# Kernel optimization log

Measured on AMD Instinct MI355X. Metric: run time of the kernel, lower is better.

Reference implementation:

```python
import jax, jax.numpy as jnp
import numpy as np

MAX_SHIFT = 4.0  # init max_shift; stored shifts are pre-divided by it
Q = 3            # Maclaurin order


def setup_inputs() -> dict:
    key = jax.random.key(0)
    k1, k2, k3, k4 = jax.random.split(key, 4)
    x = jax.random.normal(k1, (16, 64, 112, 112), jnp.float32)
    # weights: (out_channels, q*in_channels, k, k)
    weights = jax.random.normal(k2, (128, 192, 3, 3), jnp.float32) * 0.05
    bias = jax.random.normal(k3, (128,), jnp.float32) * 0.05
    # stored shifts buffer: uniform(-max_shift, max_shift) then /= max_shift -> [-1, 1]
    shifts = jax.random.uniform(k4, (64, 2), jnp.float32, -1.0, 1.0)
    return {"x": x, "weights": weights, "bias": bias, "shifts": shifts}


def _shift_one_channel(xc, sx, sy):
    """Bilinear translate one channel by (sx, sy) pixels, zero padding.
    Equivalent to F.affine_grid(identity + [sx/(W/2), sy/(H/2)]) + grid_sample
    (align_corners=False): out[n, i, j] = x[n, i + sy, j + sx] (bilinear).
    xc: (N, H, W)."""
    N, H, W = xc.shape
    jx = jnp.arange(W, dtype=xc.dtype) + sx  # sampled x coord per output col
    iy = jnp.arange(H, dtype=xc.dtype) + sy  # sampled y coord per output row
    x0f = jnp.floor(jx)
    y0f = jnp.floor(iy)
    wx = jx - x0f  # (W,)
    wy = iy - y0f  # (H,)
    x0 = x0f.astype(jnp.int32)
    y0 = y0f.astype(jnp.int32)

    def gather(yi, xi):
        vy = (yi >= 0) & (yi < H)
        vx = (xi >= 0) & (xi < W)
        yc = jnp.clip(yi, 0, H - 1)
        xcl = jnp.clip(xi, 0, W - 1)
        v = xc[:, yc, :][:, :, xcl]  # (N, H, W)
        return v * (vy[:, None] & vx[None, :]).astype(xc.dtype)

    return ((1 - wy)[:, None] * (1 - wx)[None, :] * gather(y0, x0)
            + (1 - wy)[:, None] * wx[None, :] * gather(y0, x0 + 1)
            + wy[:, None] * (1 - wx)[None, :] * gather(y0 + 1, x0)
            + wy[:, None] * wx[None, :] * gather(y0 + 1, x0 + 1))


def reference(x, weights, bias, shifts):
    s = shifts * MAX_SHIFT  # pixel shifts, (C_in, 2) = (sx, sy)
    # per-channel bilinear shift (vmap over channel axis)
    shifted = jax.vmap(_shift_one_channel, in_axes=(1, 0, 0), out_axes=1)(
        x, s[:, 0], s[:, 1])  # (N, C, H, W)
    # Maclaurin powers concatenated along channels: (N, q*C, H, W)
    y = jnp.concatenate([shifted ** i for i in range(1, Q + 1)], axis=1)
    out = jax.lax.conv_general_dilated(
        y, weights, window_strides=(1, 1), padding=[(1, 1), (1, 1)],
        dimension_numbers=("NCHW", "OIHW", "NCHW"))
    return out + bias[None, :, None, None]
```

## Files before the change

kernel.cpp:

```cpp
#include <hip/hip_runtime.h>
#include <hip/hip_bf16.h>

typedef __bf16 bf16x8 __attribute__((ext_vector_type(8)));
typedef float  f32x4  __attribute__((ext_vector_type(4)));

#define H_DIM 112
#define W_DIM 112
#define CIN 64
#define CMID 192
#define COUT 128
#define NB 16

__device__ __forceinline__ void dma16(const void* g, void* l) {
    __builtin_amdgcn_global_load_lds(
        (const __attribute__((address_space(1))) unsigned*)g,
        (__attribute__((address_space(3))) unsigned*)l, 16, 0, 0);
}

__global__ __launch_bounds__(256) void repack_w_kernel(
    const float* __restrict__ w, __hip_bfloat16* __restrict__ wr)
{
    int idx = blockIdx.x * 256 + threadIdx.x;
    if (idx < 9 * COUT * CMID) {
        int ci  = idx % CMID;
        int t   = idx / CMID;
        int co  = t % COUT;
        int khw = t / COUT;
        wr[idx] = __float2bfloat16(w[(co * CMID + ci) * 9 + khw]);
    }
}

__global__ __launch_bounds__(256) void shift_pow_kernel(
    const float* __restrict__ x, const float* __restrict__ shifts,
    __hip_bfloat16* __restrict__ y)
{
    __shared__ __align__(16) float xs[64 * 116];
    __shared__ __align__(16) __hip_bfloat16 tile[112 * 104];
    __shared__ float4 prm[32];

    const int tid = threadIdx.x;
    const int h   = blockIdx.x;
    const int cb  = blockIdx.y * 32;
    const int n   = blockIdx.z;

    if (tid < 32) {
        float sx = shifts[2 * (cb + tid)]     * 4.0f;
        float sy = shifts[2 * (cb + tid) + 1] * 4.0f;
        float fx = floorf(sx), fy = floorf(sy);
        prm[tid] = make_float4(fx, fy, sx - fx, sy - fy);
    }
    __syncthreads();

    #pragma unroll
    for (int k = 0; k < 7; ++k) {
        int i     = k * 256 + tid;
        int rowid = i / 28;
        int part  = i - rowid * 28;
        int c = rowid >> 1, t = rowid & 1;
        int iy = (int)prm[c].y;
        int r  = h + iy + t;
        bool valid = (unsigned)r < (unsigned)H_DIM;
        int rr = min(max(r, 0), H_DIM - 1);
        float4 v = ((const float4*)(
            x + ((size_t)(n * CIN + cb + c) * H_DIM + rr) * W_DIM))[part];
        if (!valid) v = make_float4(0.f, 0.f, 0.f, 0.f);
        *(float4*)&xs[rowid * 116 + part * 4] = v;
    }
    __syncthreads();

    #pragma unroll
    for (int k = 0; k < 14; ++k) {
        int i  = k * 256 + tid;
        int c  = i / 112;
        int px = i - c * 112;
        float4 p = prm[c];
        int ix = (int)p.x;
        float wx = p.z, wy = p.w;
        int q0 = px + ix, q1 = q0 + 1;
        float f0 = ((unsigned)q0 < (unsigned)W_DIM) ? 1.f : 0.f;
        float f1 = ((unsigned)q1 < (unsigned)W_DIM) ? 1.f : 0.f;
        int a0 = min(max(q0, 0), W_DIM - 1);
        int a1 = min(max(q1, 0), W_DIM - 1);
        const float* r0 = &xs[(2 * c) * 116];
        const float* r1 = &xs[(2 * c + 1) * 116];
        float top = (1.f - wx) * f0 * r0[a0] + wx * f1 * r0[a1];
        float bot = (1.f - wx) * f0 * r1[a0] + wx * f1 * r1[a1];
        float v  = (1.f - wy) * top + wy * bot;
        float v2 = v * v, v3 = v2 * v;
        __hip_bfloat16* tp = &tile[px * 104];
        tp[c]      = __float2bfloat16(v);
        tp[c + 32] = __float2bfloat16(v2);
        tp[c + 64] = __float2bfloat16(v3);
    }
    __syncthreads();

    const float4* tl4 = (const float4*)tile;
    float4* yo4 = (float4*)(y + ((size_t)(n * H_DIM + h) * W_DIM) * CMID);
    const int cbd4 = cb >> 3;
    #pragma unroll
    for (int k = 0; k < 6; ++k) {
        int i = k * 256 + tid;
        if (i < 1344) {
            int px  = i / 12;
            int cp4 = i - px * 12;
            int chunk = cp4 >> 2, e4 = cp4 & 3;
            yo4[px * 24 + chunk * 8 + cbd4 + e4] = tl4[px * 13 + cp4];
        }
    }
}

#define YSTR_E 104
#define BUF_E  12288

__global__ __launch_bounds__(256, 3) void conv_kernel(
    const __bf16* __restrict__ y,
    const __bf16* __restrict__ wr,
    const float* __restrict__ bias,
    float* __restrict__ out)
{
    __shared__ __align__(16) __bf16 ybuf[2][BUF_E];

    const int tid  = threadIdx.x;
    const int lane = tid & 63;
    const int wid  = tid >> 6;
    const int m    = lane & 15;
    const int quad = lane >> 4;

    const int h = blockIdx.x;
    const int n = blockIdx.y;

    if (tid < 208) {
        int b    = tid >= 104;
        int r    = tid - b * 104;
        int slot = (r >= 52) ? 113 : 0;
        int dw   = (r >= 52) ? r - 52 : r;
        ((unsigned*)&ybuf[b][0])[slot * 52 + dw] = 0u;
    }

    int dj[6];
    #pragma unroll
    for (int j = 0; j < 6; ++j) {
        int t = 4 * j + wid;
        int o = 208 + 1024 * t + 16 * lane;
        int slot = o / 208;
        int rem  = o - slot * 208;
        dj[j] = (t < 23 && rem < 192 && slot <= 112)
                    ? ((slot - 1) * 384 + rem) : -1;
    }

    f32x4 acc[2][7];
    #pragma unroll
    for (int mt = 0; mt < 2; ++mt)
        #pragma unroll
        for (int nt = 0; nt < 7; ++nt)
            #pragma unroll
            for (int r = 0; r < 4; ++r) acc[mt][nt][r] = 0.0f;

    const char* ybase = (const char*)y + (size_t)n * (H_DIM * W_DIM * CMID * 2);

    const int f = (h == 0)         ? 2 : 0;
    const int l = (h == H_DIM - 1) ? 3 : 5;

    {
        int row = h + (f >> 1) - 1, half = f & 1;
        const char* src = ybase + (size_t)row * (W_DIM * CMID * 2) + half * 192;
        char* lb = (char*)&ybuf[0][0];
        #pragma unroll
        for (int j = 0; j < 6; ++j) {
            int t = 4 * j + wid;
            if (dj[j] >= 0) dma16(src + dj[j], lb + 208 + 1024 * t);
        }
    }
    __syncthreads();

    int buf = 0;
    for (int s = f; s <= l; ++s) {
        if (s < l) {
            int row = h + ((s + 1) >> 1) - 1, half = (s + 1) & 1;
            const char* src = ybase + (size_t)row * (W_DIM * CMID * 2) + half * 192;
            char* lb = (char*)&ybuf[buf ^ 1][0];
            #pragma unroll
            for (int j = 0; j < 6; ++j) {
                int t = 4 * j + wid;
                if (dj[j] >= 0) dma16(src + dj[j], lb + 208 + 1024 * t);
            }
        }

        const int kh = s >> 1, half = s & 1;
        const __bf16* lbase = &ybuf[buf][m * YSTR_E + quad * 8];
        #pragma unroll
        for (int c3 = 0; c3 < 3; ++c3) {
            const int ci = half * 96 + c3 * 32 + quad * 8;
            bf16x8 af[3][2];
            #pragma unroll
            for (int kw = 0; kw < 3; ++kw)
                #pragma unroll
                for (int mt = 0; mt < 2; ++mt)
                    af[kw][mt] = *(const bf16x8*)(
                        wr + (size_t)((kh * 3 + kw) * COUT + wid * 32 + mt * 16 + m) * CMID + ci);
            #pragma unroll
            for (int kw = 0; kw < 3; ++kw) {
                bf16x8 bfr[7];
                #pragma unroll
                for (int nt = 0; nt < 7; ++nt)
                    bfr[nt] = *(const bf16x8*)(lbase + (nt * 16 + kw) * YSTR_E + c3 * 32);
                #pragma unroll
                for (int nt = 0; nt < 7; ++nt) {
                    acc[0][nt] = __builtin_amdgcn_mfma_f32_16x16x32_bf16(
                        af[kw][0], bfr[nt], acc[0][nt], 0, 0, 0);
                    acc[1][nt] = __builtin_amdgcn_mfma_f32_16x16x32_bf16(
                        af[kw][1], bfr[nt], acc[1][nt], 0, 0, 0);
                }
            }
        }
        __syncthreads();
        buf ^= 1;
    }

    #pragma unroll
    for (int mt = 0; mt < 2; ++mt) {
        const int co0 = wid * 32 + mt * 16 + quad * 4;
        float bv[4];
        #pragma unroll
        for (int rr = 0; rr < 4; ++rr) bv[rr] = bias[co0 + rr];
        #pragma unroll
        for (int nt = 0; nt < 7; ++nt) {
            int j = nt * 16 + m;
            #pragma unroll
            for (int rr = 0; rr < 4; ++rr) {
                out[(((size_t)n * COUT + co0 + rr) * H_DIM + h) * W_DIM + j] =
                    acc[mt][nt][rr] + bv[rr];
            }
        }
    }
}

extern "C" void kernel_launch(void* const* d_in, const int* in_sizes, int n_in,
                              void* d_out, int out_size, void* d_ws, size_t ws_size,
                              hipStream_t stream) {
    const float* x      = (const float*)d_in[0];
    const float* w      = (const float*)d_in[1];
    const float* bias   = (const float*)d_in[2];
    const float* shifts = (const float*)d_in[3];
    float* out = (float*)d_out;

    __hip_bfloat16* y  = (__hip_bfloat16*)d_ws;
    __hip_bfloat16* wr = (__hip_bfloat16*)((char*)d_ws + 77070336);

    repack_w_kernel<<<dim3((9 * COUT * CMID + 255) / 256), 256, 0, stream>>>(w, wr);
    shift_pow_kernel<<<dim3(H_DIM, 2, NB), 256, 0, stream>>>(x, shifts, y);
    conv_kernel<<<dim3(H_DIM, NB), 256, 0, stream>>>(
        (const __bf16*)y, (const __bf16*)wr, bias, out);
}
```

Measured before the change: 293.6 us.

## Software-pipeline LDS fragment loads with MFMA and remap blocks across XCDs

The conv inner loop now loads all 18 weight fragments up front and double-buffers the B-fragment LDS reads, prefetching the next (c3,kw) group while the current group's MFMAs run. sched_group_barrier hints interleave the ds_reads with the MFMAs. Launch bounds drop from 3 to 2 waves per EU minimum to make room for the larger register footprint. The grid is flattened and swizzled so consecutive rows of the same image land on the same XCD for L2 reuse. The cost is lower occupancy from the extra registers.

```diff
diff --git a/kernel.cpp b/kernel.cpp
--- a/kernel.cpp
+++ b/kernel.cpp
@@ -112,7 +112,34 @@
 #define YSTR_E 104
 #define BUF_E  12288
 
-__global__ __launch_bounds__(256, 3) void conv_kernel(
+#define CONV_GROUP(G, CUR, NXT) do {                                          \
+    const int c3_ = (G) / 3, kw_ = (G) % 3;                                   \
+    if ((G) < 8) {                                                            \
+        const int c3n_ = ((G) + 1) / 3, kwn_ = ((G) + 1) % 3;                 \
+        _Pragma("unroll")                                                     \
+        for (int nt = 0; nt < 7; ++nt)                                        \
+            NXT[nt] = *(const bf16x8*)(lbase +                                \
+                (nt * 16 + kwn_) * YSTR_E + c3n_ * 32);                       \
+    }                                                                         \
+    _Pragma("unroll")                                                         \
+    for (int nt = 0; nt < 7; ++nt) {                                          \
+        acc[0][nt] = __builtin_amdgcn_mfma_f32_16x16x32_bf16(                 \
+            af[c3_][kw_][0], CUR[nt], acc[0][nt], 0, 0, 0);                   \
+        acc[1][nt] = __builtin_amdgcn_mfma_f32_16x16x32_bf16(                 \
+            af[c3_][kw_][1], CUR[nt], acc[1][nt], 0, 0, 0);                   \
+    }                                                                         \
+    if ((G) < 8) {                                                            \
+        _Pragma("unroll")                                                     \
+        for (int k_ = 0; k_ < 7; ++k_) {                                      \
+            __builtin_amdgcn_sched_group_barrier(0x100, 1, 0);   \
+            __builtin_amdgcn_sched_group_barrier(0x008, 2, 0);    \
+        }                                                                     \
+    } else {                                                                  \
+        __builtin_amdgcn_sched_group_barrier(0x008, 14, 0);                   \
+    }                                                                         \
+} while (0)
+
+__global__ __launch_bounds__(256, 2) void conv_kernel(
     const __bf16* __restrict__ y,
     const __bf16* __restrict__ wr,
     const float* __restrict__ bias,
@@ -126,8 +153,10 @@
     const int m    = lane & 15;
     const int quad = lane >> 4;
 
-    const int h = blockIdx.x;
-    const int n = blockIdx.y;
+    const int bid = blockIdx.x;
+    const int id  = (bid & 7) * 224 + (bid >> 3);
+    const int n   = id / H_DIM;
+    const int h   = id - n * H_DIM;
 
     if (tid < 208) {
         int b    = tid >= 104;
@@ -188,31 +217,34 @@
 
         const int kh = s >> 1, half = s & 1;
         const __bf16* lbase = &ybuf[buf][m * YSTR_E + quad * 8];
-        #pragma unroll
-        for (int c3 = 0; c3 < 3; ++c3) {
-            const int ci = half * 96 + c3 * 32 + quad * 8;
-            bf16x8 af[3][2];
+
+        bf16x8 af[3][3][2];
+        #pragma unroll
+        for (int c3 = 0; c3 < 3; ++c3)
             #pragma unroll
             for (int kw = 0; kw < 3; ++kw)
                 #pragma unroll
                 for (int mt = 0; mt < 2; ++mt)
-                    af[kw][mt] = *(const bf16x8*)(
-                        wr + (size_t)((kh * 3 + kw) * COUT + wid * 32 + mt * 16 + m) * CMID + ci);
-            #pragma unroll
-            for (int kw = 0; kw < 3; ++kw) {
-                bf16x8 bfr[7];
-                #pragma unroll
-                for (int nt = 0; nt < 7; ++nt)
-                    bfr[nt] = *(const bf16x8*)(lbase + (nt * 16 + kw) * YSTR_E + c3 * 32);
-                #pragma unroll
-                for (int nt = 0; nt < 7; ++nt) {
-                    acc[0][nt] = __builtin_amdgcn_mfma_f32_16x16x32_bf16(
-                        af[kw][0], bfr[nt], acc[0][nt], 0, 0, 0);
-                    acc[1][nt] = __builtin_amdgcn_mfma_f32_16x16x32_bf16(
-                        af[kw][1], bfr[nt], acc[1][nt], 0, 0, 0);
-                }
-            }
-        }
+                    af[c3][kw][mt] = *(const bf16x8*)(
+                        wr + (size_t)((kh * 3 + kw) * COUT + wid * 32 + mt * 16 + m) * CMID
+                           + half * 96 + c3 * 32 + quad * 8);
+
+        bf16x8 bA[7], bB[7];
+        #pragma unroll
+        for (int nt = 0; nt < 7; ++nt)
+            bA[nt] = *(const bf16x8*)(lbase + (nt * 16 + 0) * YSTR_E + 0 * 32);
+        __builtin_amdgcn_sched_group_barrier(0x100, 7, 0);
+
+        CONV_GROUP(0, bA, bB);
+        CONV_GROUP(1, bB, bA);
+        CONV_GROUP(2, bA, bB);
+        CONV_GROUP(3, bB, bA);
+        CONV_GROUP(4, bA, bB);
+        CONV_GROUP(5, bB, bA);
+        CONV_GROUP(6, bA, bB);
+        CONV_GROUP(7, bB, bA);
+        CONV_GROUP(8, bA, bB);
+
         __syncthreads();
         buf ^= 1;
     }
@@ -249,6 +281,6 @@
 
     repack_w_kernel<<<dim3((9 * COUT * CMID + 255) / 256), 256, 0, stream>>>(w, wr);
     shift_pow_kernel<<<dim3(H_DIM, 2, NB), 256, 0, stream>>>(x, shifts, y);
-    conv_kernel<<<dim3(H_DIM, NB), 256, 0, stream>>>(
+    conv_kernel<<<dim3(H_DIM * NB), 256, 0, stream>>>(
         (const __bf16*)y, (const __bf16*)wr, bias, out);
 }
```

Result: faster. 287.5 us (-2.1%).
